# Kernel optimization log

Measured on AMD Instinct MI355X. Metric: run time of the kernel, lower is better.

The kernel has to match this reference:

```python
import jax, jax.numpy as jnp
import numpy as np

CR = 0.8
THRESH_FACTOR = 0.05
BN_EPS = 1e-5
NEG_SLOPE = 0.2

@jax.custom_vjp
def ternary(weight, pos, neg):
    # TWN-style ternarization: thresh = f * max|W|
    t = THRESH_FACTOR * jnp.max(jnp.abs(weight))
    pos_i = (weight > t).astype(weight.dtype)
    neg_i = (weight < -t).astype(weight.dtype)
    return pos * pos_i + neg * neg_i

def _tern_fwd(weight, pos, neg):
    t = THRESH_FACTOR * jnp.max(jnp.abs(weight))
    pos_i = (weight > t).astype(weight.dtype)
    neg_i = (weight < -t).astype(weight.dtype)
    return pos * pos_i + neg * neg_i, (pos_i, neg_i, pos, neg)

def _tern_bwd(res, g):
    # matches torch Function_ternary.backward (STE-style)
    pos_i, neg_i, pos, neg = res
    pruned = 1.0 - pos_i - neg_i
    grad_w = pos * g * pos_i + g * pruned + neg * g * neg_i
    return grad_w, jnp.mean(g * pos_i), jnp.mean(g * neg_i)

ternary.defvjp(_tern_fwd, _tern_bwd)

def setup_inputs() -> dict:
    key = jax.random.key(0)
    ks = jax.random.split(key, 6)
    B, Cin, H, W = 32, 256, 64, 64
    Cout, K = 512, 4
    return {
        "x": jax.random.normal(ks[0], (B, Cin, H, W), jnp.float32),
        "weight": jax.random.normal(ks[1], (Cout, Cin, K, K), jnp.float32) * 0.05,
        "pos": jax.random.uniform(ks[2], (), jnp.float32),
        "neg": -jax.random.uniform(ks[3], (), jnp.float32),
        "sal_w": jax.random.normal(ks[4], (Cout, Cin), jnp.float32) * 0.05,
        "sal_b": jax.random.normal(ks[5], (Cout,), jnp.float32) * 0.01,
        "gamma": jnp.ones((Cout,), jnp.float32),
        "beta": jnp.zeros((Cout,), jnp.float32),
    }

def reference(x, weight, pos, neg, sal_w, sal_b, gamma, beta):
    Cout = weight.shape[0]
    # FBS: per-sample channel saliency from spatially pooled |x|
    sub = jnp.mean(jnp.abs(x), axis=(2, 3))                 # [B, Cin]
    sal = jnp.abs(sub @ sal_w.T + sal_b)                    # [B, Cout]
    k = int(np.round(Cout * CR))
    thr = jax.lax.top_k(sal, k)[0][:, -1]                   # k-th largest per sample
    mask = sal * (sal > thr[:, None]).astype(x.dtype)       # [B, Cout]
    # ternary-quantized conv, stride 2, pad 1 (hardcoded in source)
    tw = ternary(weight, pos, neg)
    y = jax.lax.conv_general_dilated(
        x, tw, window_strides=(2, 2), padding=[(1, 1), (1, 1)],
        dimension_numbers=("NCHW", "OIHW", "NCHW"))          # [B, Cout, 32, 32]
    y = mask[:, :, None, None] * y
    # BatchNorm2d (training-mode batch statistics, eps=1e-5)
    mu = jnp.mean(y, axis=(0, 2, 3), keepdims=True)
    var = jnp.var(y, axis=(0, 2, 3), keepdims=True)
    y = (y - mu) * jax.lax.rsqrt(var + BN_EPS)
    y = y * gamma[None, :, None, None] + beta[None, :, None, None]
    # LeakyReLU(0.2)
    return jnp.where(y > 0, y, NEG_SLOPE * y)
```

## Files before the change

### kernel.cpp

```cpp
#include <hip/hip_runtime.h>
#include <stdint.h>

typedef __attribute__((ext_vector_type(8))) short short8;
typedef __attribute__((ext_vector_type(4))) float f32x4;
typedef __attribute__((ext_vector_type(4))) uint32_t u32x4;
typedef __attribute__((ext_vector_type(4))) unsigned short u16x4;

#define K_TOP 410

#define WS_ABSMAX 0
#define WS_GSUM   1024
#define WS_GSQ    3072
#define WS_SCALE  5120
#define WS_SHIFT  7168
#define WS_SUB    16384
#define WS_MASK   65536
#define WS_BMAT   131072

__device__ __forceinline__ unsigned short f2bf(float f) {
  uint32_t u = __float_as_uint(f);
  u += 0x7fffu + ((u >> 16) & 1u);
  return (unsigned short)(u >> 16);
}

__device__ __forceinline__ uint32_t pkbf(float a, float b) {
  uint32_t r;
  asm("v_cvt_pk_bf16_f32 %0, %1, %2" : "=v"(r) : "v"(a), "v"(b));
  return r;
}

__global__ void k_sub(const float* __restrict__ x, float* __restrict__ sub) {
  int bid = blockIdx.x;
  const f32x4* xp = (const f32x4*)(x + (size_t)bid * 4096);
  int t = threadIdx.x;
  float s = 0.f;
#pragma unroll
  for (int i = 0; i < 4; ++i) {
    f32x4 v = xp[t + i * 256];
    s += fabsf(v.x) + fabsf(v.y) + fabsf(v.z) + fabsf(v.w);
  }
#pragma unroll
  for (int off = 32; off > 0; off >>= 1) s += __shfl_xor(s, off);
  __shared__ float red[4];
  if ((t & 63) == 0) red[t >> 6] = s;
  __syncthreads();
  if (t == 0) sub[bid] = (red[0] + red[1] + red[2] + red[3]) * (1.f / 4096.f);
}

__global__ void k_wmax(const float* __restrict__ w, unsigned int* __restrict__ wsmax) {
  int t = blockIdx.x * 256 + threadIdx.x;
  const f32x4* wp = (const f32x4*)w;
  float m = 0.f;
#pragma unroll
  for (int i = 0; i < 8; ++i) {
    f32x4 v = wp[t + i * 65536];
    m = fmaxf(m, fmaxf(fmaxf(fabsf(v.x), fabsf(v.y)), fmaxf(fabsf(v.z), fabsf(v.w))));
  }
#pragma unroll
  for (int off = 32; off > 0; off >>= 1) m = fmaxf(m, __shfl_xor(m, off));
  __shared__ float red[4];
  if ((threadIdx.x & 63) == 0) red[threadIdx.x >> 6] = m;
  __syncthreads();
  if (threadIdx.x == 0) {
    m = fmaxf(fmaxf(red[0], red[1]), fmaxf(red[2], red[3]));
    atomicMax(wsmax, __float_as_uint(m));
  }
}

__global__ void k_mask(const float* __restrict__ sub, const float* __restrict__ salw,
                       const float* __restrict__ salb, float* __restrict__ mask) {
  int b = blockIdx.x, n = threadIdx.x;
  __shared__ float subs[256];
  __shared__ float sals[512];
  __shared__ float thr_s;
  if (n < 256) subs[n] = sub[b * 256 + n];
  __syncthreads();
  float acc = salb[n];
#pragma unroll 4
  for (int c = 0; c < 256; ++c) acc += subs[c] * salw[n * 256 + c];
  float sal = fabsf(acc);
  sals[n] = sal;
  __syncthreads();
  int gt = 0, eq = 0;
  for (int j = 0; j < 512; ++j) {
    float v = sals[j];
    gt += (v > sal);
    eq += (v == sal);
  }
  if (gt < K_TOP && gt + eq >= K_TOP) thr_s = sal;
  __syncthreads();
  mask[b * 512 + n] = (sal > thr_s) ? sal : 0.f;
}

__global__ void k_quant(const float* __restrict__ w, const unsigned int* __restrict__ wsmax,
                        const float* __restrict__ posp, const float* __restrict__ negp,
                        unsigned short* __restrict__ bmat2) {
  int id = blockIdx.x * 256 + threadIdx.x;
  int c = id & 2047;
  int ktq = (id >> 11) & 63;
  int ntq = id >> 17;
  int n = c >> 3, sp = c & 7;
  int s = sp ^ (n & 7);
  int cout = ntq * 256 + n;
  const float* src = w + (size_t)cout * 4096 + ktq * 64 + s * 8;
  float thr = 0.05f * __uint_as_float(*wsmax);
  unsigned short bp = f2bf(*posp), bn = f2bf(*negp);
  f32x4 a = *(const f32x4*)src;
  f32x4 bq = *(const f32x4*)(src + 4);
  u16x4 q0, q1;
  q0.x = a.x > thr ? bp : (a.x < -thr ? bn : (unsigned short)0);
  q0.y = a.y > thr ? bp : (a.y < -thr ? bn : (unsigned short)0);
  q0.z = a.z > thr ? bp : (a.z < -thr ? bn : (unsigned short)0);
  q0.w = a.w > thr ? bp : (a.w < -thr ? bn : (unsigned short)0);
  q1.x = bq.x > thr ? bp : (bq.x < -thr ? bn : (unsigned short)0);
  q1.y = bq.y > thr ? bp : (bq.y < -thr ? bn : (unsigned short)0);
  q1.z = bq.z > thr ? bp : (bq.z < -thr ? bn : (unsigned short)0);
  q1.w = bq.w > thr ? bp : (bq.w < -thr ? bn : (unsigned short)0);
  ((u16x4*)bmat2)[id * 2]     = q0;
  ((u16x4*)bmat2)[id * 2 + 1] = q1;
}

__launch_bounds__(512, 2)
__global__ void k_gemm(const float* __restrict__ x, const unsigned short* __restrict__ bmat2,
                       const float* __restrict__ mask, float* __restrict__ out,
                       float* __restrict__ gsum, float* __restrict__ gsq) {
  __shared__ __align__(16) unsigned short xsL[2][36 * 32 * 8];
  __shared__ __align__(16) unsigned short bsL[2][2048 * 8];

  int tid = threadIdx.x;
  int lane = tid & 63, wid = tid >> 6;
  int wm = wid >> 2, wn = wid & 3;
  int g = lane >> 4, lr = lane & 15;

  int wg = blockIdx.x;
  int nt = wg >> 7, mt = wg & 127;
  int b = mt >> 2, OH0 = (mt & 3) * 8;
  const size_t xb = (size_t)b * 256 * 4096;

  int jA = tid & 15, riA = tid >> 4;
  int c2A = riA / 9, rpA = riA - c2A * 9;
  int ihA = 2 * (OH0 + rpA) - 1;
  bool vA0 = (unsigned)ihA < 64u, vA1 = (unsigned)(ihA + 1) < 64u;
  const float* pA = x + xb + (size_t)c2A * 4096 + (long)ihA * 64 + 4 * jA;
  bool hasB = (wid < 4) && (lane < 16);
  int riB = 32 + wid, jB = lane & 15;
  int rpB = riB - 27;
  int ihB = 2 * (OH0 + rpB) - 1;
  bool vB0 = (unsigned)ihB < 64u, vB1 = (unsigned)(ihB + 1) < 64u;
  const float* pB = x + xb + (size_t)3 * 4096 + (long)ihB * 64 + 4 * jB;

  f32x4 acc[8][4];
#pragma unroll
  for (int i = 0; i < 8; ++i)
#pragma unroll
    for (int j = 0; j < 4; ++j) acc[i][j] = (f32x4){0.f, 0.f, 0.f, 0.f};

  auto z4 = []() { return (f32x4){0.f, 0.f, 0.f, 0.f}; };

  auto wtask = [&](int buf, int rowidx, int j, f32x4 v0, f32x4 v1) {
    float pw0 = __shfl_up(v0.w, 1);  if (j == 0)  pw0 = 0.f;
    float nx0 = __shfl_down(v0.x, 1); if (j == 15) nx0 = 0.f;
    float pw1 = __shfl_up(v1.w, 1);  if (j == 0)  pw1 = 0.f;
    float nx1 = __shfl_down(v1.x, 1); if (j == 15) nx1 = 0.f;
    uint32_t a0 = pkbf(pw0, v0.x), b0 = pkbf(v0.y, v0.z), c0 = pkbf(v0.w, nx0);
    uint32_t a1 = pkbf(pw1, v1.x), b1 = pkbf(v1.y, v1.z), c1 = pkbf(v1.w, nx1);
    u32x4* dst = (u32x4*)&xsL[buf][0];
    dst[rowidx * 32 + j]      = (u32x4){a0, b0, a1, b1};
    dst[rowidx * 32 + 16 + j] = (u32x4){b0, c0, b1, c1};
  };
  auto stageB = [&](int buf, int kt) {
    size_t gbase = (size_t)(nt * 64 + kt) * 2048 * 8;
    int wbase = tid & ~63;
#pragma unroll
    for (int q = 0; q < 4; ++q) {
      __builtin_amdgcn_global_load_lds(
          (const uint32_t*)(bmat2 + gbase + (size_t)(q * 512 + tid) * 8),
          (uint32_t*)&bsL[buf][(size_t)(q * 512 + wbase) * 8], 16, 0, 0);
    }
  };

  union UF { u32x4 u; short8 s; };

  {
    f32x4 a0 = vA0 ? *(const f32x4*)pA : z4();
    f32x4 a1 = vA1 ? *(const f32x4*)(pA + 64) : z4();
    f32x4 c0 = z4(), c1 = z4();
    if (hasB) {
      c0 = vB0 ? *(const f32x4*)pB : z4();
      c1 = vB1 ? *(const f32x4*)(pB + 64) : z4();
    }
    stageB(0, 0);
    wtask(0, riA, jA, a0, a1);
    if (hasB) wtask(0, riB, jB, c0, c1);
    asm volatile("s_waitcnt vmcnt(0) lgkmcnt(0)" ::: "memory");
    __builtin_amdgcn_s_barrier();
    __builtin_amdgcn_sched_barrier(0);
  }

  for (int kt = 0; kt < 64; ++kt) {
    int cur = kt & 1, nxt = cur ^ 1;
    bool pre = (kt < 63);

    f32x4 a0, a1, c0, c1;
    if (pre) {
      const float* p0 = pA + (size_t)(kt + 1) * 16384;
      a0 = vA0 ? *(const f32x4*)p0 : z4();
      a1 = vA1 ? *(const f32x4*)(p0 + 64) : z4();
      if (hasB) {
        const float* p1 = pB + (size_t)(kt + 1) * 16384;
        c0 = vB0 ? *(const f32x4*)p1 : z4();
        c1 = vB1 ? *(const f32x4*)(p1 + 64) : z4();
      }
      stageB(nxt, kt + 1);
    }

    const u32x4* xp4 = (const u32x4*)&xsL[cur][0];
    const u32x4* bp4 = (const u32x4*)&bsL[cur][0];
#pragma unroll
    for (int kk = 0; kk < 2; ++kk) {
      UF bf[4];
#pragma unroll
      for (int ni = 0; ni < 4; ++ni) {
        int nloc = wn * 64 + ni * 16 + lr;
        bf[ni].u = bp4[nloc * 8 + ((4 * kk + g) ^ (nloc & 7))];
      }
      UF af[8];
#pragma unroll
      for (int mi = 0; mi < 8; ++mi) {
        int rowidx = (2 * kk + (g >> 1)) * 9 + wm * 4 + (mi >> 1) + (g & 1);
        int ow = ((mi & 1) << 4) + lr;
        af[mi].u = xp4[rowidx * 32 + (ow >> 1) + ((ow & 1) << 4)];
      }
      __builtin_amdgcn_s_setprio(1);
#pragma unroll
      for (int mi = 0; mi < 8; ++mi)
#pragma unroll
        for (int ni = 0; ni < 4; ++ni)
          acc[mi][ni] = __builtin_amdgcn_mfma_f32_16x16x32_bf16(af[mi].s, bf[ni].s, acc[mi][ni], 0, 0, 0);
      __builtin_amdgcn_s_setprio(0);
      if (kk == 0) __builtin_amdgcn_s_barrier();
    }

    if (pre) {
      wtask(nxt, riA, jA, a0, a1);
      if (hasB) wtask(nxt, riB, jB, c0, c1);
    }
    asm volatile("s_waitcnt vmcnt(0) lgkmcnt(0)" ::: "memory");
    __builtin_amdgcn_s_barrier();
    __builtin_amdgcn_sched_barrier(0);
  }

  float msk[4];
#pragma unroll
  for (int ni = 0; ni < 4; ++ni)
    msk[ni] = mask[b * 512 + nt * 256 + wn * 64 + ni * 16 + lr];

  float psum[4] = {0.f, 0.f, 0.f, 0.f}, psq[4] = {0.f, 0.f, 0.f, 0.f};
#pragma unroll
  for (int ni = 0; ni < 4; ++ni) {
    int n = nt * 256 + wn * 64 + ni * 16 + lr;
    float* op = out + (size_t)b * 524288 + (size_t)n * 1024 + OH0 * 32 + wm * 128 + g * 4;
#pragma unroll
    for (int mi = 0; mi < 8; ++mi) {
      f32x4 a = acc[mi][ni] * msk[ni];
      psum[ni] += a.x + a.y + a.z + a.w;
      psq[ni] += a.x * a.x + a.y * a.y + a.z * a.z + a.w * a.w;
      *(f32x4*)(op + mi * 16) = a;
    }
  }
#pragma unroll
  for (int ni = 0; ni < 4; ++ni) {
    float s = psum[ni], q = psq[ni];
    s += __shfl_xor(s, 16); s += __shfl_xor(s, 32);
    q += __shfl_xor(q, 16); q += __shfl_xor(q, 32);
    if (g == 0) {
      int n = nt * 256 + wn * 64 + ni * 16 + lr;
      atomicAdd(&gsum[n], s);
      atomicAdd(&gsq[n], q);
    }
  }
}

__global__ void k_bnprep(const float* __restrict__ gsum, const float* __restrict__ gsq,
                         const float* __restrict__ gamma, const float* __restrict__ beta,
                         float* __restrict__ scale, float* __restrict__ shift) {
  int n = threadIdx.x;
  float mu = gsum[n] * (1.f / 32768.f);
  float var = gsq[n] * (1.f / 32768.f) - mu * mu;
  float a = gamma[n] * rsqrtf(var + 1e-5f);
  scale[n] = a;
  shift[n] = beta[n] - mu * a;
}

__global__ void k_bn(float* __restrict__ y, const float* __restrict__ scale,
                     const float* __restrict__ shift) {
  int t = blockIdx.x * 256 + threadIdx.x;
  f32x4* yp = (f32x4*)y;
#pragma unroll
  for (int i = 0; i < 8; ++i) {
    int idx = t + i * 524288;
    int n = (idx >> 8) & 511;
    f32x4 v = yp[idx];
    float a = scale[n], sh = shift[n];
    v = v * a + sh;
    v.x = v.x > 0.f ? v.x : 0.2f * v.x;
    v.y = v.y > 0.f ? v.y : 0.2f * v.y;
    v.z = v.z > 0.f ? v.z : 0.2f * v.z;
    v.w = v.w > 0.f ? v.w : 0.2f * v.w;
    yp[idx] = v;
  }
}

extern "C" void kernel_launch(void* const* d_in, const int* in_sizes, int n_in,
                              void* d_out, int out_size, void* d_ws, size_t ws_size,
                              hipStream_t stream) {
  const float* x     = (const float*)d_in[0];
  const float* w     = (const float*)d_in[1];
  const float* pos   = (const float*)d_in[2];
  const float* neg   = (const float*)d_in[3];
  const float* salw  = (const float*)d_in[4];
  const float* salb  = (const float*)d_in[5];
  const float* gamma = (const float*)d_in[6];
  const float* beta  = (const float*)d_in[7];
  float* out = (float*)d_out;
  char* ws = (char*)d_ws;

  unsigned int* absmax = (unsigned int*)(ws + WS_ABSMAX);
  float* gsum  = (float*)(ws + WS_GSUM);
  float* gsq   = (float*)(ws + WS_GSQ);
  float* scale = (float*)(ws + WS_SCALE);
  float* shift = (float*)(ws + WS_SHIFT);
  float* sub   = (float*)(ws + WS_SUB);
  float* mask  = (float*)(ws + WS_MASK);
  unsigned short* bmat2 = (unsigned short*)(ws + WS_BMAT);

  hipMemsetAsync(ws, 0, 5120, stream);

  k_sub<<<8192, 256, 0, stream>>>(x, sub);
  k_wmax<<<256, 256, 0, stream>>>(w, absmax);
  k_mask<<<32, 512, 0, stream>>>(sub, salw, salb, mask);
  k_quant<<<1024, 256, 0, stream>>>(w, absmax, pos, neg, bmat2);
  k_gemm<<<256, 512, 0, stream>>>(x, bmat2, mask, out, gsum, gsq);
  k_bnprep<<<1, 512, 0, stream>>>(gsum, gsq, gamma, beta, scale, shift);
  k_bn<<<2048, 256, 0, stream>>>(out, scale, shift);
}
```

Measured before the change: 419.4 us.

## Fuse whole pipeline into one cooperative kernel with grid syncs and register-resident BN

```diff
diff --git a/kernel.cpp b/kernel.cpp
--- a/kernel.cpp
+++ b/kernel.cpp
@@ -1,5 +1,8 @@
 #include <hip/hip_runtime.h>
+#include <hip/hip_cooperative_groups.h>
 #include <stdint.h>
+
+namespace cg = cooperative_groups;
 
 typedef __attribute__((ext_vector_type(8))) short short8;
 typedef __attribute__((ext_vector_type(4))) float f32x4;
@@ -8,14 +11,14 @@
 
 #define K_TOP 410
 
-#define WS_ABSMAX 0
-#define WS_GSUM   1024
-#define WS_GSQ    3072
 #define WS_SCALE  5120
 #define WS_SHIFT  7168
+#define WS_WPART  9216
 #define WS_SUB    16384
 #define WS_MASK   65536
 #define WS_BMAT   131072
+#define WS_PSUM   (131072 + 4194304)
+#define WS_PSQ    (131072 + 4194304 + 262144)
 
 __device__ __forceinline__ unsigned short f2bf(float f) {
   uint32_t u = __float_as_uint(f);
@@ -29,111 +32,127 @@
   return r;
 }
 
-__global__ void k_sub(const float* __restrict__ x, float* __restrict__ sub) {
-  int bid = blockIdx.x;
-  const f32x4* xp = (const f32x4*)(x + (size_t)bid * 4096);
-  int t = threadIdx.x;
-  float s = 0.f;
-#pragma unroll
-  for (int i = 0; i < 4; ++i) {
-    f32x4 v = xp[t + i * 256];
-    s += fabsf(v.x) + fabsf(v.y) + fabsf(v.z) + fabsf(v.w);
-  }
-#pragma unroll
-  for (int off = 32; off > 0; off >>= 1) s += __shfl_xor(s, off);
-  __shared__ float red[4];
-  if ((t & 63) == 0) red[t >> 6] = s;
-  __syncthreads();
-  if (t == 0) sub[bid] = (red[0] + red[1] + red[2] + red[3]) * (1.f / 4096.f);
-}
-
-__global__ void k_wmax(const float* __restrict__ w, unsigned int* __restrict__ wsmax) {
-  int t = blockIdx.x * 256 + threadIdx.x;
-  const f32x4* wp = (const f32x4*)w;
-  float m = 0.f;
-#pragma unroll
-  for (int i = 0; i < 8; ++i) {
-    f32x4 v = wp[t + i * 65536];
-    m = fmaxf(m, fmaxf(fmaxf(fabsf(v.x), fabsf(v.y)), fmaxf(fabsf(v.z), fabsf(v.w))));
-  }
-#pragma unroll
-  for (int off = 32; off > 0; off >>= 1) m = fmaxf(m, __shfl_xor(m, off));
-  __shared__ float red[4];
-  if ((threadIdx.x & 63) == 0) red[threadIdx.x >> 6] = m;
-  __syncthreads();
-  if (threadIdx.x == 0) {
-    m = fmaxf(fmaxf(red[0], red[1]), fmaxf(red[2], red[3]));
-    atomicMax(wsmax, __float_as_uint(m));
-  }
-}
-
-__global__ void k_mask(const float* __restrict__ sub, const float* __restrict__ salw,
-                       const float* __restrict__ salb, float* __restrict__ mask) {
-  int b = blockIdx.x, n = threadIdx.x;
-  __shared__ float subs[256];
-  __shared__ float sals[512];
-  __shared__ float thr_s;
-  if (n < 256) subs[n] = sub[b * 256 + n];
-  __syncthreads();
-  float acc = salb[n];
-#pragma unroll 4
-  for (int c = 0; c < 256; ++c) acc += subs[c] * salw[n * 256 + c];
-  float sal = fabsf(acc);
-  sals[n] = sal;
-  __syncthreads();
-  int gt = 0, eq = 0;
-  for (int j = 0; j < 512; ++j) {
-    float v = sals[j];
-    gt += (v > sal);
-    eq += (v == sal);
-  }
-  if (gt < K_TOP && gt + eq >= K_TOP) thr_s = sal;
-  __syncthreads();
-  mask[b * 512 + n] = (sal > thr_s) ? sal : 0.f;
-}
-
-__global__ void k_quant(const float* __restrict__ w, const unsigned int* __restrict__ wsmax,
-                        const float* __restrict__ posp, const float* __restrict__ negp,
-                        unsigned short* __restrict__ bmat2) {
-  int id = blockIdx.x * 256 + threadIdx.x;
-  int c = id & 2047;
-  int ktq = (id >> 11) & 63;
-  int ntq = id >> 17;
-  int n = c >> 3, sp = c & 7;
-  int s = sp ^ (n & 7);
-  int cout = ntq * 256 + n;
-  const float* src = w + (size_t)cout * 4096 + ktq * 64 + s * 8;
-  float thr = 0.05f * __uint_as_float(*wsmax);
-  unsigned short bp = f2bf(*posp), bn = f2bf(*negp);
-  f32x4 a = *(const f32x4*)src;
-  f32x4 bq = *(const f32x4*)(src + 4);
-  u16x4 q0, q1;
-  q0.x = a.x > thr ? bp : (a.x < -thr ? bn : (unsigned short)0);
-  q0.y = a.y > thr ? bp : (a.y < -thr ? bn : (unsigned short)0);
-  q0.z = a.z > thr ? bp : (a.z < -thr ? bn : (unsigned short)0);
-  q0.w = a.w > thr ? bp : (a.w < -thr ? bn : (unsigned short)0);
-  q1.x = bq.x > thr ? bp : (bq.x < -thr ? bn : (unsigned short)0);
-  q1.y = bq.y > thr ? bp : (bq.y < -thr ? bn : (unsigned short)0);
-  q1.z = bq.z > thr ? bp : (bq.z < -thr ? bn : (unsigned short)0);
-  q1.w = bq.w > thr ? bp : (bq.w < -thr ? bn : (unsigned short)0);
-  ((u16x4*)bmat2)[id * 2]     = q0;
-  ((u16x4*)bmat2)[id * 2 + 1] = q1;
-}
-
-__launch_bounds__(512, 2)
-__global__ void k_gemm(const float* __restrict__ x, const unsigned short* __restrict__ bmat2,
-                       const float* __restrict__ mask, float* __restrict__ out,
-                       float* __restrict__ gsum, float* __restrict__ gsq) {
-  __shared__ __align__(16) unsigned short xsL[2][36 * 32 * 8];
-  __shared__ __align__(16) unsigned short bsL[2][2048 * 8];
+__global__ __launch_bounds__(512, 2)
+void k_fused(const float* __restrict__ x, const float* __restrict__ w,
+             const float* __restrict__ posp, const float* __restrict__ negp,
+             const float* __restrict__ salw, const float* __restrict__ salb,
+             const float* __restrict__ gamma, const float* __restrict__ beta,
+             float* __restrict__ out, char* __restrict__ ws) {
+  __shared__ __align__(16) unsigned short xs[2][36 * 32 * 8];
+  float* Lf = (float*)&xs[0][0];
+
+  float* scaleA = (float*)(ws + WS_SCALE);
+  float* shiftA = (float*)(ws + WS_SHIFT);
+  float* wpart  = (float*)(ws + WS_WPART);
+  float* sub    = (float*)(ws + WS_SUB);
+  float* maskA  = (float*)(ws + WS_MASK);
+  unsigned short* bmat3 = (unsigned short*)(ws + WS_BMAT);
+  float* psumA  = (float*)(ws + WS_PSUM);
+  float* psqA   = (float*)(ws + WS_PSQ);
 
   int tid = threadIdx.x;
   int lane = tid & 63, wid = tid >> 6;
-  int wm = wid >> 2, wn = wid & 3;
+  int wg = blockIdx.x;
+  cg::grid_group grid = cg::this_grid();
+
+  {
+#pragma unroll
+    for (int rr = 0; rr < 4; ++rr) {
+      int row = wg * 32 + wid * 4 + rr;
+      const f32x4* rp = (const f32x4*)(x + (size_t)row * 4096);
+      float s = 0.f;
+#pragma unroll
+      for (int i = 0; i < 16; ++i) {
+        f32x4 v = rp[lane + i * 64];
+        s += fabsf(v.x) + fabsf(v.y) + fabsf(v.z) + fabsf(v.w);
+      }
+#pragma unroll
+      for (int o = 1; o < 64; o <<= 1) s += __shfl_xor(s, o);
+      if (lane == 0) sub[row] = s * (1.f / 4096.f);
+    }
+    const f32x4* wp = (const f32x4*)w + (size_t)wg * 2048;
+    float m = 0.f;
+#pragma unroll
+    for (int i = 0; i < 4; ++i) {
+      f32x4 v = wp[tid + i * 512];
+      m = fmaxf(m, fmaxf(fmaxf(fabsf(v.x), fabsf(v.y)), fmaxf(fabsf(v.z), fabsf(v.w))));
+    }
+#pragma unroll
+    for (int o = 1; o < 64; o <<= 1) m = fmaxf(m, __shfl_xor(m, o));
+    if (lane == 0) Lf[wid] = m;
+    __syncthreads();
+    if (tid == 0) {
+      float mm = Lf[0];
+#pragma unroll
+      for (int i = 1; i < 8; ++i) mm = fmaxf(mm, Lf[i]);
+      wpart[wg] = mm;
+    }
+    __syncthreads();
+  }
+  grid.sync();
+
+  {
+    f32x4 wv = ((const f32x4*)wpart)[lane];
+    float m = fmaxf(fmaxf(wv.x, wv.y), fmaxf(wv.z, wv.w));
+#pragma unroll
+    for (int o = 1; o < 64; o <<= 1) m = fmaxf(m, __shfl_xor(m, o));
+    float thr = 0.05f * m;
+    unsigned short bp = f2bf(*posp), bn = f2bf(*negp);
+#pragma unroll
+    for (int q = 0; q < 2; ++q) {
+      int id = wg * 1024 + tid * 2 + q;
+      int lp = id & 63, nn = (id >> 6) & 15, kk = (id >> 10) & 1;
+      int kt = (id >> 11) & 63, nt = id >> 17;
+      int gq = lp >> 4, lrq = lp & 15;
+      int cout = nt * 256 + nn * 16 + lrq;
+      const float* src = w + (size_t)cout * 4096 + kt * 64 + kk * 32 + gq * 8;
+      f32x4 a = *(const f32x4*)src;
+      f32x4 b2 = *(const f32x4*)(src + 4);
+      u16x4 q0, q1;
+      q0.x = a.x > thr ? bp : (a.x < -thr ? bn : (unsigned short)0);
+      q0.y = a.y > thr ? bp : (a.y < -thr ? bn : (unsigned short)0);
+      q0.z = a.z > thr ? bp : (a.z < -thr ? bn : (unsigned short)0);
+      q0.w = a.w > thr ? bp : (a.w < -thr ? bn : (unsigned short)0);
+      q1.x = b2.x > thr ? bp : (b2.x < -thr ? bn : (unsigned short)0);
+      q1.y = b2.y > thr ? bp : (b2.y < -thr ? bn : (unsigned short)0);
+      q1.z = b2.z > thr ? bp : (b2.z < -thr ? bn : (unsigned short)0);
+      q1.w = b2.w > thr ? bp : (b2.w < -thr ? bn : (unsigned short)0);
+      ((u16x4*)bmat3)[(size_t)id * 2]     = q0;
+      ((u16x4*)bmat3)[(size_t)id * 2 + 1] = q1;
+    }
+    if (wg < 32) {
+      float* subs = Lf;
+      float* sals = Lf + 256;
+      float* thrp = Lf + 768;
+      if (tid < 256) subs[tid] = sub[wg * 256 + tid];
+      __syncthreads();
+      float acc = salb[tid];
+      const f32x4* swp = (const f32x4*)(salw + (size_t)tid * 256);
+#pragma unroll 4
+      for (int i = 0; i < 64; ++i) {
+        f32x4 v = swp[i];
+        acc += subs[4 * i] * v.x + subs[4 * i + 1] * v.y +
+               subs[4 * i + 2] * v.z + subs[4 * i + 3] * v.w;
+      }
+      float sal = fabsf(acc);
+      sals[tid] = sal;
+      __syncthreads();
+      int gt = 0, eq = 0;
+      for (int j = 0; j < 512; ++j) {
+        float v = sals[j];
+        gt += (v > sal); eq += (v == sal);
+      }
+      if (gt < K_TOP && gt + eq >= K_TOP) *thrp = sal;
+      __syncthreads();
+      maskA[wg * 512 + tid] = (sal > *thrp) ? sal : 0.f;
+      __syncthreads();
+    }
+  }
+  grid.sync();
+
+  int nt = wg >> 7, mt = wg & 127;
+  int wm = wid >> 1, wn = wid & 1;
   int g = lane >> 4, lr = lane & 15;
-
-  int wg = blockIdx.x;
-  int nt = wg >> 7, mt = wg & 127;
   int b = mt >> 2, OH0 = (mt & 3) * 8;
   const size_t xb = (size_t)b * 256 * 4096;
 
@@ -149,37 +168,28 @@
   bool vB0 = (unsigned)ihB < 64u, vB1 = (unsigned)(ihB + 1) < 64u;
   const float* pB = x + xb + (size_t)3 * 4096 + (long)ihB * 64 + 4 * jB;
 
-  f32x4 acc[8][4];
-#pragma unroll
-  for (int i = 0; i < 8; ++i)
-#pragma unroll
-    for (int j = 0; j < 4; ++j) acc[i][j] = (f32x4){0.f, 0.f, 0.f, 0.f};
+  f32x4 acc[4][8];
+#pragma unroll
+  for (int i = 0; i < 4; ++i)
+#pragma unroll
+    for (int j = 0; j < 8; ++j) acc[i][j] = (f32x4){0.f, 0.f, 0.f, 0.f};
 
   auto z4 = []() { return (f32x4){0.f, 0.f, 0.f, 0.f}; };
-
   auto wtask = [&](int buf, int rowidx, int j, f32x4 v0, f32x4 v1) {
-    float pw0 = __shfl_up(v0.w, 1);  if (j == 0)  pw0 = 0.f;
+    float pw0 = __shfl_up(v0.w, 1);   if (j == 0)  pw0 = 0.f;
     float nx0 = __shfl_down(v0.x, 1); if (j == 15) nx0 = 0.f;
-    float pw1 = __shfl_up(v1.w, 1);  if (j == 0)  pw1 = 0.f;
+    float pw1 = __shfl_up(v1.w, 1);   if (j == 0)  pw1 = 0.f;
     float nx1 = __shfl_down(v1.x, 1); if (j == 15) nx1 = 0.f;
     uint32_t a0 = pkbf(pw0, v0.x), b0 = pkbf(v0.y, v0.z), c0 = pkbf(v0.w, nx0);
     uint32_t a1 = pkbf(pw1, v1.x), b1 = pkbf(v1.y, v1.z), c1 = pkbf(v1.w, nx1);
-    u32x4* dst = (u32x4*)&xsL[buf][0];
+    u32x4* dst = (u32x4*)&xs[buf][0];
     dst[rowidx * 32 + j]      = (u32x4){a0, b0, a1, b1};
     dst[rowidx * 32 + 16 + j] = (u32x4){b0, c0, b1, c1};
   };
-  auto stageB = [&](int buf, int kt) {
-    size_t gbase = (size_t)(nt * 64 + kt) * 2048 * 8;
-    int wbase = tid & ~63;
-#pragma unroll
-    for (int q = 0; q < 4; ++q) {
-      __builtin_amdgcn_global_load_lds(
-          (const uint32_t*)(bmat2 + gbase + (size_t)(q * 512 + tid) * 8),
-          (uint32_t*)&bsL[buf][(size_t)(q * 512 + wbase) * 8], 16, 0, 0);
-    }
-  };
-
+
+  const u32x4* bm4 = (const u32x4*)bmat3;
   union UF { u32x4 u; short8 s; };
+  UF b0f[8], b1f[8];
 
   {
     f32x4 a0 = vA0 ? *(const f32x4*)pA : z4();
@@ -189,7 +199,9 @@
       c0 = vB0 ? *(const f32x4*)pB : z4();
       c1 = vB1 ? *(const f32x4*)(pB + 64) : z4();
     }
-    stageB(0, 0);
+    int cb = (nt * 64 * 2) * 1024 + (wn * 8) * 64 + lane;
+#pragma unroll
+    for (int ni = 0; ni < 8; ++ni) b0f[ni].u = bm4[cb + ni * 64];
     wtask(0, riA, jA, a0, a1);
     if (hasB) wtask(0, riB, jB, c0, c1);
     asm volatile("s_waitcnt vmcnt(0) lgkmcnt(0)" ::: "memory");
@@ -211,103 +223,139 @@
         c0 = vB0 ? *(const f32x4*)p1 : z4();
         c1 = vB1 ? *(const f32x4*)(p1 + 64) : z4();
       }
-      stageB(nxt, kt + 1);
-    }
-
-    const u32x4* xp4 = (const u32x4*)&xsL[cur][0];
-    const u32x4* bp4 = (const u32x4*)&bsL[cur][0];
-#pragma unroll
-    for (int kk = 0; kk < 2; ++kk) {
-      UF bf[4];
-#pragma unroll
-      for (int ni = 0; ni < 4; ++ni) {
-        int nloc = wn * 64 + ni * 16 + lr;
-        bf[ni].u = bp4[nloc * 8 + ((4 * kk + g) ^ (nloc & 7))];
-      }
-      UF af[8];
-#pragma unroll
-      for (int mi = 0; mi < 8; ++mi) {
-        int rowidx = (2 * kk + (g >> 1)) * 9 + wm * 4 + (mi >> 1) + (g & 1);
+    }
+    {
+      int cb = ((nt * 64 + kt) * 2 + 1) * 1024 + (wn * 8) * 64 + lane;
+#pragma unroll
+      for (int ni = 0; ni < 8; ++ni) b1f[ni].u = bm4[cb + ni * 64];
+    }
+    const u32x4* xp4 = (const u32x4*)&xs[cur][0];
+    {
+      UF af[4];
+#pragma unroll
+      for (int mi = 0; mi < 4; ++mi) {
+        int rowidx = (g >> 1) * 9 + wm * 2 + (mi >> 1) + (g & 1);
         int ow = ((mi & 1) << 4) + lr;
         af[mi].u = xp4[rowidx * 32 + (ow >> 1) + ((ow & 1) << 4)];
       }
       __builtin_amdgcn_s_setprio(1);
 #pragma unroll
-      for (int mi = 0; mi < 8; ++mi)
-#pragma unroll
-        for (int ni = 0; ni < 4; ++ni)
-          acc[mi][ni] = __builtin_amdgcn_mfma_f32_16x16x32_bf16(af[mi].s, bf[ni].s, acc[mi][ni], 0, 0, 0);
+      for (int mi = 0; mi < 4; ++mi)
+#pragma unroll
+        for (int ni = 0; ni < 8; ++ni)
+          acc[mi][ni] = __builtin_amdgcn_mfma_f32_16x16x32_bf16(af[mi].s, b0f[ni].s, acc[mi][ni], 0, 0, 0);
       __builtin_amdgcn_s_setprio(0);
-      if (kk == 0) __builtin_amdgcn_s_barrier();
-    }
-
+    }
+    __builtin_amdgcn_s_barrier();
+    if (pre) {
+      int cb = ((nt * 64 + kt + 1) * 2) * 1024 + (wn * 8) * 64 + lane;
+#pragma unroll
+      for (int ni = 0; ni < 8; ++ni) b0f[ni].u = bm4[cb + ni * 64];
+    }
+    {
+      UF af[4];
+#pragma unroll
+      for (int mi = 0; mi < 4; ++mi) {
+        int rowidx = (2 + (g >> 1)) * 9 + wm * 2 + (mi >> 1) + (g & 1);
+        int ow = ((mi & 1) << 4) + lr;
+        af[mi].u = xp4[rowidx * 32 + (ow >> 1) + ((ow & 1) << 4)];
+      }
+      __builtin_amdgcn_s_setprio(1);
+#pragma unroll
+      for (int mi = 0; mi < 4; ++mi)
+#pragma unroll
+        for (int ni = 0; ni < 8; ++ni)
+          acc[mi][ni] = __builtin_amdgcn_mfma_f32_16x16x32_bf16(af[mi].s, b1f[ni].s, acc[mi][ni], 0, 0, 0);
+      __builtin_amdgcn_s_setprio(0);
+    }
     if (pre) {
       wtask(nxt, riA, jA, a0, a1);
       if (hasB) wtask(nxt, riB, jB, c0, c1);
     }
-    asm volatile("s_waitcnt vmcnt(0) lgkmcnt(0)" ::: "memory");
+    asm volatile("s_waitcnt lgkmcnt(0)" ::: "memory");
     __builtin_amdgcn_s_barrier();
     __builtin_amdgcn_sched_barrier(0);
   }
 
-  float msk[4];
-#pragma unroll
-  for (int ni = 0; ni < 4; ++ni)
-    msk[ni] = mask[b * 512 + nt * 256 + wn * 64 + ni * 16 + lr];
-
-  float psum[4] = {0.f, 0.f, 0.f, 0.f}, psq[4] = {0.f, 0.f, 0.f, 0.f};
-#pragma unroll
-  for (int ni = 0; ni < 4; ++ni) {
-    int n = nt * 256 + wn * 64 + ni * 16 + lr;
-    float* op = out + (size_t)b * 524288 + (size_t)n * 1024 + OH0 * 32 + wm * 128 + g * 4;
-#pragma unroll
-    for (int mi = 0; mi < 8; ++mi) {
+  float msk[8];
+#pragma unroll
+  for (int ni = 0; ni < 8; ++ni)
+    msk[ni] = maskA[b * 512 + nt * 256 + wn * 128 + ni * 16 + lr];
+
+  float ps[8], pq[8];
+#pragma unroll
+  for (int ni = 0; ni < 8; ++ni) {
+    ps[ni] = 0.f; pq[ni] = 0.f;
+#pragma unroll
+    for (int mi = 0; mi < 4; ++mi) {
       f32x4 a = acc[mi][ni] * msk[ni];
-      psum[ni] += a.x + a.y + a.z + a.w;
-      psq[ni] += a.x * a.x + a.y * a.y + a.z * a.z + a.w * a.w;
-      *(f32x4*)(op + mi * 16) = a;
-    }
-  }
-#pragma unroll
-  for (int ni = 0; ni < 4; ++ni) {
-    float s = psum[ni], q = psq[ni];
-    s += __shfl_xor(s, 16); s += __shfl_xor(s, 32);
-    q += __shfl_xor(q, 16); q += __shfl_xor(q, 32);
-    if (g == 0) {
-      int n = nt * 256 + wn * 64 + ni * 16 + lr;
-      atomicAdd(&gsum[n], s);
-      atomicAdd(&gsq[n], q);
-    }
-  }
-}
-
-__global__ void k_bnprep(const float* __restrict__ gsum, const float* __restrict__ gsq,
-                         const float* __restrict__ gamma, const float* __restrict__ beta,
-                         float* __restrict__ scale, float* __restrict__ shift) {
-  int n = threadIdx.x;
-  float mu = gsum[n] * (1.f / 32768.f);
-  float var = gsq[n] * (1.f / 32768.f) - mu * mu;
-  float a = gamma[n] * rsqrtf(var + 1e-5f);
-  scale[n] = a;
-  shift[n] = beta[n] - mu * a;
-}
-
-__global__ void k_bn(float* __restrict__ y, const float* __restrict__ scale,
-                     const float* __restrict__ shift) {
-  int t = blockIdx.x * 256 + threadIdx.x;
-  f32x4* yp = (f32x4*)y;
-#pragma unroll
-  for (int i = 0; i < 8; ++i) {
-    int idx = t + i * 524288;
-    int n = (idx >> 8) & 511;
-    f32x4 v = yp[idx];
-    float a = scale[n], sh = shift[n];
-    v = v * a + sh;
-    v.x = v.x > 0.f ? v.x : 0.2f * v.x;
-    v.y = v.y > 0.f ? v.y : 0.2f * v.y;
-    v.z = v.z > 0.f ? v.z : 0.2f * v.z;
-    v.w = v.w > 0.f ? v.w : 0.2f * v.w;
-    yp[idx] = v;
+      acc[mi][ni] = a;
+      ps[ni] += a.x + a.y + a.z + a.w;
+      pq[ni] += a.x * a.x + a.y * a.y + a.z * a.z + a.w * a.w;
+    }
+  }
+#pragma unroll
+  for (int ni = 0; ni < 8; ++ni) {
+    ps[ni] += __shfl_xor(ps[ni], 16); ps[ni] += __shfl_xor(ps[ni], 32);
+    pq[ni] += __shfl_xor(pq[ni], 16); pq[ni] += __shfl_xor(pq[ni], 32);
+  }
+  __syncthreads();
+  if (g == 0) {
+#pragma unroll
+    for (int ni = 0; ni < 8; ++ni) {
+      int ch = wn * 128 + ni * 16 + lr;
+      Lf[wm * 256 + ch]        = ps[ni];
+      Lf[1024 + wm * 256 + ch] = pq[ni];
+    }
+  }
+  __syncthreads();
+  if (tid < 256) {
+    float bs = Lf[tid] + Lf[256 + tid] + Lf[512 + tid] + Lf[768 + tid];
+    float bq = Lf[1024 + tid] + Lf[1280 + tid] + Lf[1536 + tid] + Lf[1792 + tid];
+    psumA[(size_t)(nt * 128 + mt) * 256 + tid] = bs;
+    psqA [(size_t)(nt * 128 + mt) * 256 + tid] = bq;
+  }
+  grid.sync();
+
+  {
+    int c = wg * 2 + (tid >> 8);
+    int ntc = c >> 8, ch = c & 255, s = tid & 255;
+    float v1 = 0.f, v2 = 0.f;
+    if (s < 128) {
+      v1 = psumA[(size_t)(ntc * 128 + s) * 256 + ch];
+      v2 = psqA [(size_t)(ntc * 128 + s) * 256 + ch];
+    }
+#pragma unroll
+    for (int o = 1; o < 64; o <<= 1) { v1 += __shfl_xor(v1, o); v2 += __shfl_xor(v2, o); }
+    if (lane == 0) { Lf[2048 + wid] = v1; Lf[2056 + wid] = v2; }
+    __syncthreads();
+    if ((tid & 255) == 0) {
+      int base = (tid >> 8) * 4;
+      float S = Lf[2048 + base] + Lf[2049 + base] + Lf[2050 + base] + Lf[2051 + base];
+      float Q = Lf[2056 + base] + Lf[2057 + base] + Lf[2058 + base] + Lf[2059 + base];
+      float mu = S * (1.f / 32768.f);
+      float var = Q * (1.f / 32768.f) - mu * mu;
+      float sc = gamma[c] * rsqrtf(var + 1e-5f);
+      scaleA[c] = sc;
+      shiftA[c] = beta[c] - mu * sc;
+    }
+  }
+  grid.sync();
+
+#pragma unroll
+  for (int ni = 0; ni < 8; ++ni) {
+    int n = nt * 256 + wn * 128 + ni * 16 + lr;
+    float sc = scaleA[n], sh = shiftA[n];
+    float* op = out + (size_t)b * 524288 + (size_t)n * 1024 + OH0 * 32 + wm * 64 + g * 4;
+#pragma unroll
+    for (int mi = 0; mi < 4; ++mi) {
+      f32x4 v = acc[mi][ni] * sc + sh;
+      v.x = v.x > 0.f ? v.x : 0.2f * v.x;
+      v.y = v.y > 0.f ? v.y : 0.2f * v.y;
+      v.z = v.z > 0.f ? v.z : 0.2f * v.z;
+      v.w = v.w > 0.f ? v.w : 0.2f * v.w;
+      *(f32x4*)(op + mi * 16) = v;
+    }
   }
 }
 
@@ -325,22 +373,7 @@
   float* out = (float*)d_out;
   char* ws = (char*)d_ws;
 
-  unsigned int* absmax = (unsigned int*)(ws + WS_ABSMAX);
-  float* gsum  = (float*)(ws + WS_GSUM);
-  float* gsq   = (float*)(ws + WS_GSQ);
-  float* scale = (float*)(ws + WS_SCALE);
-  float* shift = (float*)(ws + WS_SHIFT);
-  float* sub   = (float*)(ws + WS_SUB);
-  float* mask  = (float*)(ws + WS_MASK);
-  unsigned short* bmat2 = (unsigned short*)(ws + WS_BMAT);
-
-  hipMemsetAsync(ws, 0, 5120, stream);
-
-  k_sub<<<8192, 256, 0, stream>>>(x, sub);
-  k_wmax<<<256, 256, 0, stream>>>(w, absmax);
-  k_mask<<<32, 512, 0, stream>>>(sub, salw, salb, mask);
-  k_quant<<<1024, 256, 0, stream>>>(w, absmax, pos, neg, bmat2);
-  k_gemm<<<256, 512, 0, stream>>>(x, bmat2, mask, out, gsum, gsq);
-  k_bnprep<<<1, 512, 0, stream>>>(gsum, gsq, gamma, beta, scale, shift);
-  k_bn<<<2048, 256, 0, stream>>>(out, scale, shift);
+  void* args[] = { (void*)&x, (void*)&w, (void*)&pos, (void*)&neg, (void*)&salw,
+                   (void*)&salb, (void*)&gamma, (void*)&beta, (void*)&out, (void*)&ws };
+  hipLaunchCooperativeKernel((void*)k_fused, dim3(256), dim3(512), args, 0, stream);
 }
```

New measurement: 506.3 us. 20.7% more time.
